# Kernel tuning notes

Hardware: AMD Instinct MI355X
Metric: run time of the kernel (lower is better)

## Reference

```python
import jax, jax.numpy as jnp
import numpy as np

B, S = 2, 2048
NUM_HEADS, NUM_KV_HEADS, HEAD_DIM = 32, 8, 128
HIDDEN = NUM_HEADS * HEAD_DIM  # 4096
Q_SIZE = NUM_HEADS * HEAD_DIM
KV_SIZE = NUM_KV_HEADS * HEAD_DIM
ROPE_THETA = 100000.0
SCALE = HEAD_DIM ** -0.5


def setup_inputs() -> dict:
    key = jax.random.key(0)
    k1, k2, k3, k4, k5 = jax.random.split(key, 5)
    T = B * S
    return {
        "hidden_states": jax.random.normal(k1, (T, HIDDEN), jnp.float32) * 0.02,
        "positions": jnp.arange(T, dtype=jnp.int64) % S,  # per-sequence positions
        "w_qkv": jax.random.normal(k2, (HIDDEN, Q_SIZE + 2 * KV_SIZE), jnp.float32) * 0.02,
        "b_qkv": jax.random.normal(k3, (Q_SIZE + 2 * KV_SIZE,), jnp.float32) * 0.01,
        "w_o": jax.random.normal(k4, (Q_SIZE, HIDDEN), jnp.float32) * 0.02,
        "b_o": jax.random.normal(k5, (HIDDEN,), jnp.float32) * 0.01,
    }


def _rope_neox(x, positions):
    # x: [T, H, D]; neox style rotates the two halves of head_dim
    half = HEAD_DIM // 2
    inv_freq = 1.0 / (ROPE_THETA ** (jnp.arange(0, HEAD_DIM, 2, dtype=jnp.float32) / HEAD_DIM))
    freqs = positions.astype(jnp.float32)[:, None] * inv_freq[None, :]  # [T, D/2]
    cos = jnp.cos(freqs)[:, None, :]  # [T, 1, D/2]
    sin = jnp.sin(freqs)[:, None, :]
    x1, x2 = x[..., :half], x[..., half:]
    return jnp.concatenate([x1 * cos - x2 * sin, x2 * cos + x1 * sin], axis=-1)


def reference(hidden_states, positions, w_qkv, b_qkv, w_o, b_o):
    T = hidden_states.shape[0]
    qkv = hidden_states @ w_qkv + b_qkv  # [T, q+2kv]
    q = qkv[:, :Q_SIZE].reshape(T, NUM_HEADS, HEAD_DIM)
    k = qkv[:, Q_SIZE:Q_SIZE + KV_SIZE].reshape(T, NUM_KV_HEADS, HEAD_DIM)
    v = qkv[:, Q_SIZE + KV_SIZE:].reshape(T, NUM_KV_HEADS, HEAD_DIM)

    q = _rope_neox(q, positions)
    k = _rope_neox(k, positions)

    # reshape flattened tokens back to [B, S, ...] for causal self-attention
    q = q.reshape(B, S, NUM_HEADS, HEAD_DIM)
    k = k.reshape(B, S, NUM_KV_HEADS, HEAD_DIM)
    v = v.reshape(B, S, NUM_KV_HEADS, HEAD_DIM)

    # GQA: repeat kv heads to match query heads
    group = NUM_HEADS // NUM_KV_HEADS
    k = jnp.repeat(k, group, axis=2)  # [B, S, H, D]
    v = jnp.repeat(v, group, axis=2)

    scores = jnp.einsum("bqhd,bkhd->bhqk", q, k) * SCALE  # [B, H, S, S]
    causal = jnp.tril(jnp.ones((S, S), dtype=bool))
    scores = jnp.where(causal[None, None], scores, jnp.finfo(scores.dtype).min)
    probs = jax.nn.softmax(scores, axis=-1)
    attn = jnp.einsum("bhqk,bkhd->bqhd", probs, v)  # [B, S, H, D]

    attn = attn.reshape(T, Q_SIZE)
    return attn @ w_o + b_o  # [T, HIDDEN]
```

## Files before the change

### kernel.cpp

```cpp
#include <hip/hip_runtime.h>
#include <cstdint>
#include <math.h>

#define T_TOTAL 4096
#define S_LEN   2048
#define NH      32
#define NKV     8
#define HD      128
#define HIDDEN  4096
#define QSZ     4096
#define KVSZ    1024
#define QKV_N   6144
#define SCALE_F 0.08838834764831843f

typedef __bf16 bf16x8 __attribute__((ext_vector_type(8)));
typedef float  f32x4  __attribute__((ext_vector_type(4)));
typedef unsigned short u16;
typedef unsigned int   u32;
typedef u16 u16x8 __attribute__((ext_vector_type(8)));
typedef u16 u16x4 __attribute__((ext_vector_type(4)));

__device__ __forceinline__ u16 f2bf(float f) {
  u32 b = __float_as_uint(f);
  b += 0x7FFFu + ((b >> 16) & 1u);
  return (u16)(b >> 16);
}

__device__ __forceinline__ void async_copy16(const u16* g, u16* l) {
  __builtin_amdgcn_global_load_lds(
      (const __attribute__((address_space(1))) void*)(g),
      (__attribute__((address_space(3))) void*)(l), 16, 0, 0);
}

__global__ __launch_bounds__(256) void cast_bf16_kernel(const float4* __restrict__ in,
                                                        ushort4* __restrict__ out, int n4) {
  int i = blockIdx.x * 256 + threadIdx.x;
  if (i >= n4) return;
  float4 v = in[i];
  ushort4 o;
  o.x = f2bf(v.x); o.y = f2bf(v.y); o.z = f2bf(v.z); o.w = f2bf(v.w);
  out[i] = o;
}

__global__ __launch_bounds__(256) void transpose_cast_kernel(const float* __restrict__ in,
                                                             u16* __restrict__ out, int R, int C) {
  __shared__ float tile[32][33];
  int bx = blockIdx.x * 32;
  int by = blockIdx.y * 32;
  int tx = threadIdx.x & 31, ty = threadIdx.x >> 5;
  for (int i = ty; i < 32; i += 8)
    tile[i][tx] = in[(size_t)(by + i) * C + bx + tx];
  __syncthreads();
  for (int i = ty; i < 32; i += 8)
    out[(size_t)(bx + i) * R + by + tx] = f2bf(tile[tx][i]);
}

__global__ __launch_bounds__(512) void gemm_pipe_kernel(const u16* __restrict__ A,
                                                        const u16* __restrict__ Bt,
                                                        const float* __restrict__ bias,
                                                        float* __restrict__ C,
                                                        int M, int N, int K, int nbn) {
  __shared__ u16 lds[2][2][8192];
  const int tid  = threadIdx.x;
  const int lane = tid & 63, wave = tid >> 6;
  const int quad = lane >> 4, l16 = lane & 15;
  const int wm = (wave >> 2) * 128;
  const int wn = (wave & 3) * 64;

  const int cpx = gridDim.x >> 3;
  const int logical = (blockIdx.x & 7) * cpx + (blockIdx.x >> 3);
  const int bm = logical / nbn, bn = logical % nbn;

  const int trow = tid >> 2;
  const int gch  = ((tid & 3) ^ ((tid >> 3) & 3)) * 8;
  const u16* gA = A  + (size_t)(bm * 256 + trow) * K + gch;
  const u16* gB = Bt + (size_t)(bn * 256 + trow) * K + gch;
  const size_t eoff = (size_t)128 * K;

  const int NT = K >> 5;
#pragma unroll
  for (int pt = 0; pt < 2; ++pt) {
    int kt = pt * 32;
    async_copy16(gA + kt,        &lds[pt][0][tid * 8]);
    async_copy16(gA + eoff + kt, &lds[pt][0][4096 + tid * 8]);
    async_copy16(gB + kt,        &lds[pt][1][tid * 8]);
    async_copy16(gB + eoff + kt, &lds[pt][1][4096 + tid * 8]);
  }

  const int sw = (quad ^ ((l16 >> 1) & 3)) * 8;
  f32x4 acc[8][4] = {};
  for (int t = 0; t < NT; ++t) {
    if (t + 1 < NT) asm volatile("s_waitcnt vmcnt(4)" ::: "memory");
    else            asm volatile("s_waitcnt vmcnt(0)" ::: "memory");
    __builtin_amdgcn_s_barrier();

    const u16* sAt = lds[t & 1][0];
    const u16* sBt = lds[t & 1][1];
    bf16x8 af[8], bfr[4];
#pragma unroll
    for (int i = 0; i < 8; ++i)
      af[i] = *(const bf16x8*)&sAt[(wm + i * 16 + l16) * 32 + sw];
#pragma unroll
    for (int j = 0; j < 4; ++j)
      bfr[j] = *(const bf16x8*)&sBt[(wn + j * 16 + l16) * 32 + sw];
    asm volatile("s_waitcnt lgkmcnt(0)" ::: "memory");
    __builtin_amdgcn_s_barrier();

    if (t + 2 < NT) {
      int kt = (t + 2) * 32;
      async_copy16(gA + kt,        &lds[t & 1][0][tid * 8]);
      async_copy16(gA + eoff + kt, &lds[t & 1][0][4096 + tid * 8]);
      async_copy16(gB + kt,        &lds[t & 1][1][tid * 8]);
      async_copy16(gB + eoff + kt, &lds[t & 1][1][4096 + tid * 8]);
    }

    __builtin_amdgcn_s_setprio(1);
#pragma unroll
    for (int i = 0; i < 8; ++i)
#pragma unroll
      for (int j = 0; j < 4; ++j)
        acc[i][j] = __builtin_amdgcn_mfma_f32_16x16x32_bf16(af[i], bfr[j], acc[i][j], 0, 0, 0);
    __builtin_amdgcn_s_setprio(0);
  }

#pragma unroll
  for (int i = 0; i < 8; ++i) {
    int row0 = bm * 256 + wm + i * 16 + quad * 4;
#pragma unroll
    for (int j = 0; j < 4; ++j) {
      int col = bn * 256 + wn + j * 16 + l16;
      float bi = bias[col];
#pragma unroll
      for (int r = 0; r < 4; ++r)
        C[(size_t)(row0 + r) * N + col] = acc[i][j][r] + bi;
    }
  }
}

__global__ __launch_bounds__(256) void qk_rope_cast_kernel(const float* __restrict__ qkv,
                                                           const int* __restrict__ pos,
                                                           u16* __restrict__ Qb,
                                                           u16* __restrict__ Kb) {
  int idx = blockIdx.x * 256 + threadIdx.x;
  int t = idx / 2560;
  int rem = idx - t * 2560;
  int head = rem >> 6, i = rem & 63;
  int b = t >> 11, s = t & 2047;
  float p = (float)pos[t];
  float inv = exp2f(-(float)i * 0.25952563f);
  float f = p * inv;
  float sn, cs;
  sincosf(f, &sn, &cs);
  if (head < NH) {
    const float* src = qkv + (size_t)t * QKV_N + head * HD;
    float x1 = src[i], x2 = src[i + 64];
    u16* dst = Qb + (((size_t)(b * NH + head)) * S_LEN + s) * HD;
    dst[i]      = f2bf((x1 * cs - x2 * sn) * SCALE_F);
    dst[i + 64] = f2bf((x2 * cs + x1 * sn) * SCALE_F);
  } else {
    int kh = head - NH;
    const float* src = qkv + (size_t)t * QKV_N + QSZ + kh * HD;
    float x1 = src[i], x2 = src[i + 64];
    u16* dst = Kb + (((size_t)(b * NKV + kh)) * S_LEN + s) * HD;
    dst[i]      = f2bf(x1 * cs - x2 * sn);
    dst[i + 64] = f2bf(x2 * cs + x1 * sn);
  }
}

__global__ __launch_bounds__(256) void v_transpose_cast_kernel(const float* __restrict__ qkv,
                                                               u16* __restrict__ Vtb) {
  __shared__ float tile[32][33];
  int st = blockIdx.x * 32;
  int dt = blockIdx.y * 32;
  int bk = blockIdx.z;
  int b = bk >> 3, kvh = bk & 7;
  int tx = threadIdx.x & 31, ty = threadIdx.x >> 5;
  const float* src = qkv + (size_t)(b * S_LEN) * QKV_N + QSZ + KVSZ + kvh * HD;
  for (int i = ty; i < 32; i += 8)
    tile[i][tx] = src[(size_t)(st + i) * QKV_N + dt + tx];
  __syncthreads();
  u16* dst = Vtb + (size_t)bk * HD * S_LEN;
  for (int i = ty; i < 32; i += 8)
    dst[(size_t)(dt + i) * S_LEN + st + tx] = f2bf(tile[tx][i]);
}

__global__ __launch_bounds__(256) void flash_mfma_kernel(const u16* __restrict__ Qb,
                                                         const u16* __restrict__ Kb,
                                                         const u16* __restrict__ Vtb,
                                                         u16* __restrict__ attn) {
  const int qti = gridDim.x - 1 - blockIdx.x;
  const int h = blockIdx.y, b = blockIdx.z;
  const int kvh = h >> 2;
  const int tid = threadIdx.x;
  const int lane = tid & 63, wave = tid >> 6;
  const int quad = lane >> 4, l16 = lane & 15;

  __shared__ u16 sK[64 * 128];
  __shared__ u16 sVt[128 * 64];
  __shared__ u16 sP[4][16 * 64];

  bf16x8 qf[4];
  {
    const u16* qrow = Qb + (((size_t)(b * NH + h)) * S_LEN + (size_t)qti * 64 + wave * 16 + l16) * HD;
#pragma unroll
    for (int kc = 0; kc < 4; ++kc)
      qf[kc] = *(const bf16x8*)(qrow + kc * 32 + quad * 8);
  }

  f32x4 acc[8] = {};
  float m_r = -INFINITY;
  float l_r = 0.f;

  const u16* Kbase = Kb  + ((size_t)(b * NKV + kvh)) * S_LEN * HD;
  const u16* Vbase = Vtb + ((size_t)(b * NKV + kvh)) * HD * S_LEN;

  u16x8 kv[4], vv[4];
#pragma unroll
  for (int i = 0; i < 4; ++i) {
    int c = i * 256 + tid;
    kv[i] = *(const u16x8*)(Kbase + (size_t)(c >> 4) * HD + (c & 15) * 8);
    vv[i] = *(const u16x8*)(Vbase + (size_t)(c >> 3) * S_LEN + (c & 7) * 8);
  }

  for (int kt = 0; kt <= qti; ++kt) {
    __syncthreads();
#pragma unroll
    for (int i = 0; i < 4; ++i) {
      int c = i * 256 + tid;
      int kr = c >> 4;
      *(u16x8*)&sK[(kr * 128 + (c & 15) * 8) ^ ((kr & 7) << 3)] = kv[i];
      int vr = c >> 3;
      *(u16x8*)&sVt[(vr * 64 + (c & 7) * 8) ^ ((vr & 7) << 3)] = vv[i];
    }
    __syncthreads();

    if (kt < qti) {
#pragma unroll
      for (int i = 0; i < 4; ++i) {
        int c = i * 256 + tid;
        kv[i] = *(const u16x8*)(Kbase + (size_t)((kt + 1) * 64 + (c >> 4)) * HD + (c & 15) * 8);
        vv[i] = *(const u16x8*)(Vbase + (size_t)(c >> 3) * S_LEN + (kt + 1) * 64 + (c & 7) * 8);
      }
    }

    f32x4 s[4] = {};
#pragma unroll
    for (int kc = 0; kc < 4; ++kc) {
#pragma unroll
      for (int nb = 0; nb < 4; ++nb) {
        bf16x8 kf = *(const bf16x8*)&sK[((nb * 16 + l16) * 128 + kc * 32 + quad * 8) ^ ((l16 & 7) << 3)];
        s[nb] = __builtin_amdgcn_mfma_f32_16x16x32_bf16(kf, qf[kc], s[nb], 0, 0, 0);
      }
    }

    if (kt == qti) {
      int qloc = wave * 16 + l16;
#pragma unroll
      for (int nb = 0; nb < 4; ++nb)
#pragma unroll
        for (int r = 0; r < 4; ++r)
          if (nb * 16 + quad * 4 + r > qloc) s[nb][r] = -1e30f;
    }

    float mx = -1e30f;
#pragma unroll
    for (int nb = 0; nb < 4; ++nb)
#pragma unroll
      for (int r = 0; r < 4; ++r)
        mx = fmaxf(mx, s[nb][r]);
    mx = fmaxf(mx, __shfl_xor(mx, 16));
    mx = fmaxf(mx, __shfl_xor(mx, 32));
    float mnew = fmaxf(m_r, mx);
    float alpha = __expf(m_r - mnew);
    m_r = mnew;
    float rs = 0.f;
#pragma unroll
    for (int nb = 0; nb < 4; ++nb)
#pragma unroll
      for (int r = 0; r < 4; ++r) {
        float p = __expf(s[nb][r] - mnew);
        s[nb][r] = p;
        rs += p;
      }
    rs += __shfl_xor(rs, 16);
    rs += __shfl_xor(rs, 32);
    l_r = l_r * alpha + rs;

#pragma unroll
    for (int db = 0; db < 8; ++db)
#pragma unroll
      for (int r = 0; r < 4; ++r)
        acc[db][r] *= alpha;

    u16* sPw = sP[wave];
#pragma unroll
    for (int nb = 0; nb < 4; ++nb) {
      u16x4 pk;
#pragma unroll
      for (int r = 0; r < 4; ++r) pk[r] = f2bf(s[nb][r]);
      *(u16x4*)&sPw[(l16 * 64 + nb * 16 + quad * 4) ^ ((l16 & 7) << 3)] = pk;
    }

#pragma unroll
    for (int ch = 0; ch < 2; ++ch) {
      bf16x8 pf = *(const bf16x8*)&sPw[(l16 * 64 + ch * 32 + quad * 8) ^ ((l16 & 7) << 3)];
#pragma unroll
      for (int db = 0; db < 8; ++db) {
        bf16x8 vf = *(const bf16x8*)&sVt[((db * 16 + l16) * 64 + ch * 32 + quad * 8) ^ ((l16 & 7) << 3)];
        acc[db] = __builtin_amdgcn_mfma_f32_16x16x32_bf16(vf, pf, acc[db], 0, 0, 0);
      }
    }
  }

  float invl = 1.0f / l_r;
  __syncthreads();
  u16* sOw = &sK[wave * 2048];
#pragma unroll
  for (int db = 0; db < 8; ++db) {
    u16x4 pk;
#pragma unroll
    for (int r = 0; r < 4; ++r) pk[r] = f2bf(acc[db][r] * invl);
    *(u16x4*)&sOw[(l16 * 128 + db * 16 + quad * 4) ^ ((l16 & 7) << 3)] = pk;
  }
#pragma unroll
  for (int p = 0; p < 4; ++p) {
    int row = p * 4 + quad;
    u16x8 o = *(const u16x8*)&sOw[(row * 128 + l16 * 8) ^ ((row & 7) << 3)];
    int q = qti * 64 + wave * 16 + row;
    *(u16x8*)(attn + ((size_t)(b * S_LEN + q)) * QSZ + (size_t)h * HD + l16 * 8) = o;
  }
}

extern "C" void kernel_launch(void* const* d_in, const int* in_sizes, int n_in,
                              void* d_out, int out_size, void* d_ws, size_t ws_size,
                              hipStream_t stream) {
  const float* hidden    = (const float*)d_in[0];
  const int*   positions = (const int*)d_in[1];
  const float* w_qkv     = (const float*)d_in[2];
  const float* b_qkv     = (const float*)d_in[3];
  const float* w_o       = (const float*)d_in[4];
  const float* b_o       = (const float*)d_in[5];
  float* out = (float*)d_out;

  char* ws = (char*)d_ws;
  const size_t MB = 1024 * 1024;
  u16*   hb    = (u16*)ws;
  u16*   wqT   = (u16*)(ws + 32  * MB);
  u16*   woT   = (u16*)(ws + 80  * MB);
  float* qkv   = (float*)(ws + 112 * MB);
  u16*   attnb = (u16*)(ws + 208 * MB);
  u16*   Qb    = (u16*)ws;
  u16*   Kb    = (u16*)(ws + 32 * MB);
  u16*   Vtb   = (u16*)(ws + 40 * MB);

  cast_bf16_kernel<<<T_TOTAL * HIDDEN / 4 / 256, 256, 0, stream>>>(
      (const float4*)hidden, (ushort4*)hb, T_TOTAL * HIDDEN / 4);
  transpose_cast_kernel<<<dim3(QKV_N / 32, HIDDEN / 32), 256, 0, stream>>>(w_qkv, wqT, HIDDEN, QKV_N);
  transpose_cast_kernel<<<dim3(HIDDEN / 32, QSZ / 32), 256, 0, stream>>>(w_o, woT, QSZ, HIDDEN);
  gemm_pipe_kernel<<<dim3((T_TOTAL / 256) * (QKV_N / 256)), 512, 0, stream>>>(
      hb, wqT, b_qkv, qkv, T_TOTAL, QKV_N, HIDDEN, QKV_N / 256);
  qk_rope_cast_kernel<<<T_TOTAL * 2560 / 256, 256, 0, stream>>>(qkv, positions, Qb, Kb);
  v_transpose_cast_kernel<<<dim3(S_LEN / 32, HD / 32, 16), 256, 0, stream>>>(qkv, Vtb);
  flash_mfma_kernel<<<dim3(S_LEN / 64, NH, 2), 256, 0, stream>>>(Qb, Kb, Vtb, attnb);
  gemm_pipe_kernel<<<dim3((T_TOTAL / 256) * (HIDDEN / 256)), 512, 0, stream>>>(
      attnb, woT, b_o, out, T_TOTAL, HIDDEN, QSZ, HIDDEN / 256);
}
```

Baseline: 920.7 us.

## Use 128-row query tiles with 8 waves and lazy softmax rescaling in flash attention

The flash attention block grows from 64 to 128 query rows, run by 8 waves. Each K/V tile staged in shared memory is now reused by twice as many queries, which halves the global K/V traffic per query. Waves whose causal range ends early skip the compute on the final tile but still take part in the loads and barriers. It also adds a lazy online-softmax rescale that skips the max reduction and accumulator rescale while the new max stays within a threshold of 8. This trades fewer blocks and some idle waves for less load traffic and fewer exp/multiply operations.

```diff
diff --git a/kernel.cpp b/kernel.cpp
--- a/kernel.cpp
+++ b/kernel.cpp
@@ -184,7 +184,7 @@
     dst[(size_t)(dt + i) * S_LEN + st + tx] = f2bf(tile[tx][i]);
 }
 
-__global__ __launch_bounds__(256) void flash_mfma_kernel(const u16* __restrict__ Qb,
+__global__ __launch_bounds__(512) void flash_mfma_kernel(const u16* __restrict__ Qb,
                                                          const u16* __restrict__ Kb,
                                                          const u16* __restrict__ Vtb,
                                                          u16* __restrict__ attn) {
@@ -195,13 +195,14 @@
   const int lane = tid & 63, wave = tid >> 6;
   const int quad = lane >> 4, l16 = lane & 15;
 
-  __shared__ u16 sK[64 * 128];
-  __shared__ u16 sVt[128 * 64];
-  __shared__ u16 sP[4][16 * 64];
+  __shared__ u16 smem[24576];
+  u16* sK  = smem;
+  u16* sVt = smem + 8192;
+  u16* sPw = smem + 16384 + wave * 1024;
 
   bf16x8 qf[4];
   {
-    const u16* qrow = Qb + (((size_t)(b * NH + h)) * S_LEN + (size_t)qti * 64 + wave * 16 + l16) * HD;
+    const u16* qrow = Qb + (((size_t)(b * NH + h)) * S_LEN + (size_t)qti * 128 + wave * 16 + l16) * HD;
 #pragma unroll
     for (int kc = 0; kc < 4; ++kc)
       qf[kc] = *(const bf16x8*)(qrow + kc * 32 + quad * 8);
@@ -214,19 +215,22 @@
   const u16* Kbase = Kb  + ((size_t)(b * NKV + kvh)) * S_LEN * HD;
   const u16* Vbase = Vtb + ((size_t)(b * NKV + kvh)) * HD * S_LEN;
 
-  u16x8 kv[4], vv[4];
-#pragma unroll
-  for (int i = 0; i < 4; ++i) {
-    int c = i * 256 + tid;
+  u16x8 kv[2], vv[2];
+#pragma unroll
+  for (int i = 0; i < 2; ++i) {
+    int c = i * 512 + tid;
     kv[i] = *(const u16x8*)(Kbase + (size_t)(c >> 4) * HD + (c & 15) * 8);
     vv[i] = *(const u16x8*)(Vbase + (size_t)(c >> 3) * S_LEN + (c & 7) * 8);
   }
 
-  for (int kt = 0; kt <= qti; ++kt) {
+  const int nkt = 2 * qti + 2;
+  const int lastkt = 2 * qti + (wave >> 2);
+
+  for (int kt = 0; kt < nkt; ++kt) {
     __syncthreads();
 #pragma unroll
-    for (int i = 0; i < 4; ++i) {
-      int c = i * 256 + tid;
+    for (int i = 0; i < 2; ++i) {
+      int c = i * 512 + tid;
       int kr = c >> 4;
       *(u16x8*)&sK[(kr * 128 + (c & 15) * 8) ^ ((kr & 7) << 3)] = kv[i];
       int vr = c >> 3;
@@ -234,14 +238,16 @@
     }
     __syncthreads();
 
-    if (kt < qti) {
-#pragma unroll
-      for (int i = 0; i < 4; ++i) {
-        int c = i * 256 + tid;
+    if (kt + 1 < nkt) {
+#pragma unroll
+      for (int i = 0; i < 2; ++i) {
+        int c = i * 512 + tid;
         kv[i] = *(const u16x8*)(Kbase + (size_t)((kt + 1) * 64 + (c >> 4)) * HD + (c & 15) * 8);
         vv[i] = *(const u16x8*)(Vbase + (size_t)(c >> 3) * S_LEN + (kt + 1) * 64 + (c & 7) * 8);
       }
     }
+
+    if (kt > lastkt) continue;
 
     f32x4 s[4] = {};
 #pragma unroll
@@ -253,13 +259,14 @@
       }
     }
 
-    if (kt == qti) {
-      int qloc = wave * 16 + l16;
+    if (kt == lastkt) {
+      int qg = qti * 128 + wave * 16 + l16;
+      int k0 = kt * 64;
 #pragma unroll
       for (int nb = 0; nb < 4; ++nb)
 #pragma unroll
         for (int r = 0; r < 4; ++r)
-          if (nb * 16 + quad * 4 + r > qloc) s[nb][r] = -1e30f;
+          if (k0 + nb * 16 + quad * 4 + r > qg) s[nb][r] = -1e30f;
     }
 
     float mx = -1e30f;
@@ -268,17 +275,25 @@
 #pragma unroll
       for (int r = 0; r < 4; ++r)
         mx = fmaxf(mx, s[nb][r]);
-    mx = fmaxf(mx, __shfl_xor(mx, 16));
-    mx = fmaxf(mx, __shfl_xor(mx, 32));
-    float mnew = fmaxf(m_r, mx);
-    float alpha = __expf(m_r - mnew);
-    m_r = mnew;
+    float alpha = 1.f;
+    if (!__all(mx - m_r <= 8.f)) {
+      mx = fmaxf(mx, __shfl_xor(mx, 16));
+      mx = fmaxf(mx, __shfl_xor(mx, 32));
+      float mnew = fmaxf(m_r, mx);
+      alpha = __expf(m_r - mnew);
+      m_r = mnew;
+#pragma unroll
+      for (int db = 0; db < 8; ++db)
+#pragma unroll
+        for (int r = 0; r < 4; ++r)
+          acc[db][r] *= alpha;
+    }
     float rs = 0.f;
 #pragma unroll
     for (int nb = 0; nb < 4; ++nb)
 #pragma unroll
       for (int r = 0; r < 4; ++r) {
-        float p = __expf(s[nb][r] - mnew);
+        float p = __expf(s[nb][r] - m_r);
         s[nb][r] = p;
         rs += p;
       }
@@ -287,13 +302,6 @@
     l_r = l_r * alpha + rs;
 
 #pragma unroll
-    for (int db = 0; db < 8; ++db)
-#pragma unroll
-      for (int r = 0; r < 4; ++r)
-        acc[db][r] *= alpha;
-
-    u16* sPw = sP[wave];
-#pragma unroll
     for (int nb = 0; nb < 4; ++nb) {
       u16x4 pk;
 #pragma unroll
@@ -314,7 +322,7 @@
 
   float invl = 1.0f / l_r;
   __syncthreads();
-  u16* sOw = &sK[wave * 2048];
+  u16* sOw = &smem[wave * 2048];
 #pragma unroll
   for (int db = 0; db < 8; ++db) {
     u16x4 pk;
@@ -326,7 +334,7 @@
   for (int p = 0; p < 4; ++p) {
     int row = p * 4 + quad;
     u16x8 o = *(const u16x8*)&sOw[(row * 128 + l16 * 8) ^ ((row & 7) << 3)];
-    int q = qti * 64 + wave * 16 + row;
+    int q = qti * 128 + wave * 16 + row;
     *(u16x8*)(attn + ((size_t)(b * S_LEN + q)) * QSZ + (size_t)h * HD + l16 * 8) = o;
   }
 }
@@ -361,7 +369,7 @@
       hb, wqT, b_qkv, qkv, T_TOTAL, QKV_N, HIDDEN, QKV_N / 256);
   qk_rope_cast_kernel<<<T_TOTAL * 2560 / 256, 256, 0, stream>>>(qkv, positions, Qb, Kb);
   v_transpose_cast_kernel<<<dim3(S_LEN / 32, HD / 32, 16), 256, 0, stream>>>(qkv, Vtb);
-  flash_mfma_kernel<<<dim3(S_LEN / 64, NH, 2), 256, 0, stream>>>(Qb, Kb, Vtb, attnb);
+  flash_mfma_kernel<<<dim3(S_LEN / 128, NH, 2), 512, 0, stream>>>(Qb, Kb, Vtb, attnb);
   gemm_pipe_kernel<<<dim3((T_TOTAL / 256) * (HIDDEN / 256)), 512, 0, stream>>>(
       attnb, woT, b_o, out, T_TOTAL, HIDDEN, QSZ, HIDDEN / 256);
 }
```

New measurement: 887.7 us. 1.04x faster.
